# Performance work log

Hardware: AMD Instinct MI355X
Metric: run time of the kernel (lower is better)

The kernel has to match this reference:

```python
import jax, jax.numpy as jnp
import numpy as np
from jax import lax

B, N, C = 4, 16384, 256
NH, HD = 8, 32          # num_heads, head_dim
SR = 4                  # spatial reduction ratio
LMAX = 6144             # max per-batch query length (static pad size)
QLENS = np.array([2048, 6144, 3072, 5120], dtype=np.int32)
TQ = int(QLENS.sum())   # 16384 total ragged queries
SCALE = HD ** -0.5


def setup_inputs() -> dict:
    key = jax.random.key(0)
    ks = jax.random.split(key, 6)
    w = lambda k, s: jax.random.normal(k, s, jnp.float32) * 0.02
    return {
        "x": jax.random.normal(ks[0], (B, N, C), jnp.float32),
        "q": jax.random.normal(ks[1], (TQ, C), jnp.float32),
        "H": 128,
        "W": 128,
        "q_lengths": jnp.asarray(QLENS),
        "w_q": w(ks[2], (C, C)),        # stored [in, out] (= torch W.T)
        "w_kv": w(ks[3], (C, 2 * C)),
        "sr_w": w(ks[4], (C, C, SR, SR)),  # OIHW
        "sr_b": jnp.zeros((C,), jnp.float32),
        "ln_g": jnp.ones((C,), jnp.float32),
        "ln_b": jnp.zeros((C,), jnp.float32),
        "proj_w": w(ks[5], (C, C)),
        "proj_b": jnp.zeros((C,), jnp.float32),
    }


def reference(x, q, H, W, q_lengths, w_q, w_kv, sr_w, sr_b, ln_g, ln_b, proj_w, proj_b):
    # q projection -> per-head ragged queries [NH, TQ, HD]
    qh = (q @ w_q).reshape(TQ, NH, HD).transpose(1, 0, 2)

    # spatial reduction of KV source: conv(k=SR, stride=SR) + LayerNorm
    x_ = x.transpose(0, 2, 1).reshape(B, C, H, W)
    x_ = lax.conv_general_dilated(x_, sr_w, (SR, SR), "VALID",
                                  dimension_numbers=("NCHW", "OIHW", "NCHW"))
    x_ = x_ + sr_b[None, :, None, None]
    x_ = x_.reshape(B, C, -1).transpose(0, 2, 1)  # [B, Nkv, C]
    mu = x_.mean(-1, keepdims=True)
    var = ((x_ - mu) ** 2).mean(-1, keepdims=True)
    x_ = (x_ - mu) * lax.rsqrt(var + 1e-5) * ln_g + ln_b

    # kv projection -> [NH, B, Nkv, HD] each
    kv = (x_ @ w_kv).reshape(B, -1, 2, NH, HD)
    k = kv[:, :, 0].transpose(2, 0, 1, 3)
    v = kv[:, :, 1].transpose(2, 0, 1, 3)

    # ragged -> padded layout for the variable-length attention
    batch_ids = jnp.repeat(jnp.arange(B), q_lengths, total_repeat_length=TQ)
    offsets = jnp.cumsum(q_lengths) - q_lengths
    pos = jnp.arange(TQ) - offsets[batch_ids]
    qp = jnp.zeros((NH, B, LMAX, HD), qh.dtype).at[:, batch_ids, pos].set(qh)

    # per-batch attention over reduced keys (padded rows are discarded below)
    attn = jax.nn.softmax(jnp.einsum("hbld,hbkd->hblk", qp, k) * SCALE, axis=-1)
    op = jnp.einsum("hblk,hbkd->hbld", attn, v)

    # gather valid ragged outputs back: [NH, TQ, HD] -> [TQ, C]
    o = op[:, batch_ids, pos].transpose(1, 0, 2).reshape(TQ, C)
    return o @ proj_w + proj_b
```

## Files before the change

### kernel.cpp

```cpp
#include <hip/hip_runtime.h>
#include <hip/hip_bf16.h>


using bf16 = __hip_bfloat16;
using f32x4 = __attribute__((ext_vector_type(4))) float;
using bf16x8 = __attribute__((ext_vector_type(8))) short;

#define DEVINL __device__ __forceinline__
#define AS1 __attribute__((address_space(1)))
#define AS3 __attribute__((address_space(3)))

DEVINL f32x4 mfma16(bf16x8 a, bf16x8 b, f32x4 c) {
    return __builtin_amdgcn_mfma_f32_16x16x32_bf16(a, b, c, 0, 0, 0);
}

DEVINL unsigned short f2bf(float f) {
    union { float f; unsigned u; } x; x.f = f;
    unsigned u = x.u;
    u += 0x7fffu + ((u >> 16) & 1u);
    return (unsigned short)(u >> 16);
}

DEVINL unsigned pk_rtz(float a, float b) {
    return __builtin_amdgcn_perm(__float_as_uint(b), __float_as_uint(a), 0x07060302u);
}

DEVINL float ex2(float x) { return __builtin_amdgcn_exp2f(x); }

DEVINL void gl16(const bf16* g, bf16* l) {
    __builtin_amdgcn_global_load_lds(
        (const AS1 void*)(unsigned long long)(uintptr_t)g,
        (AS3 void*)(unsigned)(uintptr_t)l,
        16, 0, 0);
}


__global__ __launch_bounds__(256) void cast_bf16_kernel(const float* __restrict__ in,
                                                        bf16* __restrict__ out, int n8) {
    int i = blockIdx.x * 256 + threadIdx.x;
    if (i >= n8) return;
    float4 a = ((const float4*)in)[i * 2];
    float4 b = ((const float4*)in)[i * 2 + 1];
    uint4 u;
    u.x = f2bf(a.x) | ((unsigned)f2bf(a.y) << 16);
    u.y = f2bf(a.z) | ((unsigned)f2bf(a.w) << 16);
    u.z = f2bf(b.x) | ((unsigned)f2bf(b.y) << 16);
    u.w = f2bf(b.z) | ((unsigned)f2bf(b.w) << 16);
    ((uint4*)out)[i] = u;
}

__global__ __launch_bounds__(256) void im2col_kernel(const float* __restrict__ x,
                                                     bf16* __restrict__ xim) {
    int m = blockIdx.x * 256 + threadIdx.x;
    int cc8 = (m & 31) << 3;
    int dydx = (m >> 5) & 15;
    int pr = m >> 9;
    int b = pr >> 10, pi = pr & 1023;
    int ii = pi >> 5, jj = pi & 31;
    int dy = dydx >> 2, dx = dydx & 3;
    int pos = ((ii << 2) + dy) * 128 + (jj << 2) + dx;
    const float* s = &x[(size_t)((b << 14) + pos) * 256 + cc8];
    float4 a = *(const float4*)s;
    float4 c = *(const float4*)(s + 4);
    uint4 u;
    u.x = f2bf(a.x) | ((unsigned)f2bf(a.y) << 16);
    u.y = f2bf(a.z) | ((unsigned)f2bf(a.w) << 16);
    u.z = f2bf(c.x) | ((unsigned)f2bf(c.y) << 16);
    u.w = f2bf(c.z) | ((unsigned)f2bf(c.w) << 16);
    *(uint4*)&xim[(size_t)m * 8] = u;
}

__global__ __launch_bounds__(256) void transpose_cast_kernel(const float* __restrict__ in,
                                                             bf16* __restrict__ out, int K, int N) {
    int idx = blockIdx.x * 256 + threadIdx.x;
    if (idx >= K * N) return;
    int k = idx % K, n = idx / K;
    out[idx] = __float2bfloat16(in[k * N + n]);
}

__global__ __launch_bounds__(256) void conv_w_kernel(const float* __restrict__ sr_w,
                                                     bf16* __restrict__ out) {
    int idx = blockIdx.x * 256 + threadIdx.x;
    int o = idx >> 12, rest = idx & 4095, dydx = rest >> 8, c = rest & 255;
    out[idx] = __float2bfloat16(sr_w[((o << 8) + c) * 16 + dydx]);
}

template<int EMODE>
__global__ __launch_bounds__(256, 4) void gemm_kernel(
    const bf16* __restrict__ A, const bf16* __restrict__ WT,
    const float* __restrict__ bias,
    bf16* __restrict__ outb, float* __restrict__ outf, bf16* __restrict__ out2,
    int M, int N, int K, int KS)
{
    __shared__ alignas(16) bf16 As[2][64 * 64];
    __shared__ alignas(16) bf16 Bs[2][64 * 64];
    const int cpx = gridDim.x >> 3;
    const int bx = (blockIdx.x & 7) * cpx + (blockIdx.x >> 3);
    const int ntn = N >> 6;
    const int tm = bx / ntn, tn = bx % ntn;
    const int tid = threadIdx.x, lane = tid & 63, wid = tid >> 6;
    const int l15 = lane & 15, g = lane >> 4;
    const int wm = (wid >> 1) << 5, wn = (wid & 1) << 5;
    f32x4 acc[2][2] = {};

    int r_[2], cs_[2];
#pragma unroll
    for (int j = 0; j < 2; ++j) {
        int idx = (wid * 2 + j) * 64 + lane;
        r_[j] = idx >> 3;
        cs_[j] = ((idx & 7) ^ (r_[j] & 7)) << 3;
    }
    const bf16* Arow = &A[(size_t)(tm * 64) * K];
    const bf16* Brow = &WT[(size_t)(tn * 64) * K];

    const int kbeg = blockIdx.y * KS;
    const int nsteps = KS >> 6;

    auto stage = [&](int buf, int k0) {
#pragma unroll
        for (int j = 0; j < 2; ++j) {
            gl16(Arow + (size_t)r_[j] * K + (k0 + cs_[j]), &As[buf][(wid * 2 + j) * 512]);
            gl16(Brow + (size_t)r_[j] * K + (k0 + cs_[j]), &Bs[buf][(wid * 2 + j) * 512]);
        }
    };

    stage(0, kbeg);
    __syncthreads();

    for (int t = 0; t < nsteps; ++t) {
        const int buf = t & 1;
        if (t + 1 < nsteps) stage(buf ^ 1, kbeg + (t + 1) * 64);
#pragma unroll
        for (int kk = 0; kk < 2; ++kk) {
            const int sw = l15 & 7;
            const int co = ((kk * 4 + g) ^ sw) << 3;
            bf16x8 a0 = *(const bf16x8*)&As[buf][(wm + l15) * 64 + co];
            bf16x8 a1 = *(const bf16x8*)&As[buf][(wm + 16 + l15) * 64 + co];
            bf16x8 b0 = *(const bf16x8*)&Bs[buf][(wn + l15) * 64 + co];
            bf16x8 b1 = *(const bf16x8*)&Bs[buf][(wn + 16 + l15) * 64 + co];
            acc[0][0] = mfma16(a0, b0, acc[0][0]);
            acc[0][1] = mfma16(a0, b1, acc[0][1]);
            acc[1][0] = mfma16(a1, b0, acc[1][0]);
            acc[1][1] = mfma16(a1, b1, acc[1][1]);
        }
        __syncthreads();
    }

    const float qscale = 0.1767766953f * 1.4426950409f;
#pragma unroll
    for (int mi = 0; mi < 2; ++mi)
#pragma unroll
    for (int ni = 0; ni < 2; ++ni)
#pragma unroll
    for (int r = 0; r < 4; ++r) {
        int row = tm * 64 + wm + mi * 16 + g * 4 + r;
        int col = tn * 64 + wn + ni * 16 + l15;
        float v = acc[mi][ni][r];
        if constexpr (EMODE == 0) {
            outb[(size_t)row * 256 + col] = __float2bfloat16(v * qscale);
        } else if constexpr (EMODE == 1) {
            outf[(size_t)row * 256 + col] = v + bias[col];
        } else if constexpr (EMODE == 2) {
            int bb = row >> 10, key = row & 1023;
            if (col < 256) {
                int hh = col >> 5, d = col & 31;
                outb[(size_t)(((bb << 3) + hh) * 1024 + key) * 32 + d] = __float2bfloat16(v);
            } else {
                int d = col - 256;
                int c = key & 31;
                int pos = (((c >> 2) & 3) << 3) + ((c >> 4) << 2) + (c & 3);
                int keyp = (key & ~31) | pos;
                out2[(size_t)(((bb << 3) + (d >> 5)) * 32 + (d & 31)) * 1024 + keyp] =
                    __float2bfloat16(v);
            }
        } else {
            outf[((size_t)blockIdx.y * 4096 + row) * 256 + col] = v;
        }
    }
}

__global__ __launch_bounds__(256) void ln_kernel(const float* __restrict__ pp,
                                                 const float* __restrict__ cb,
                                                 const float* __restrict__ gw,
                                                 const float* __restrict__ bw,
                                                 bf16* __restrict__ out) {
    int row = blockIdx.x * 4 + (threadIdx.x >> 6);
    int lane = threadIdx.x & 63;
    const size_t base = (size_t)row * 256 + lane * 4;
    float4 v = *(const float4*)&pp[base];
#pragma unroll
    for (int s = 1; s < 4; ++s) {
        const float4 t = *(const float4*)&pp[(size_t)s * (4096 * 256) + base];
        v.x += t.x; v.y += t.y; v.z += t.z; v.w += t.w;
    }
    const float4 cbv = *(const float4*)&cb[lane * 4];
    v.x += cbv.x; v.y += cbv.y; v.z += cbv.z; v.w += cbv.w;

    float s = v.x + v.y + v.z + v.w;
#pragma unroll
    for (int m = 1; m < 64; m <<= 1) s += __shfl_xor(s, m, 64);
    float mu = s * 0.00390625f;
    float d0 = v.x - mu, d1 = v.y - mu, d2 = v.z - mu, d3 = v.w - mu;
    float qv = d0 * d0 + d1 * d1 + d2 * d2 + d3 * d3;
#pragma unroll
    for (int m = 1; m < 64; m <<= 1) qv += __shfl_xor(qv, m, 64);
    float rstd = rsqrtf(qv * 0.00390625f + 1e-5f);
    const float4 gg = *(const float4*)&gw[lane * 4];
    const float4 bb = *(const float4*)&bw[lane * 4];
    uint2 u;
    u.x = f2bf(d0 * rstd * gg.x + bb.x) | ((unsigned)f2bf(d1 * rstd * gg.y + bb.y) << 16);
    u.y = f2bf(d2 * rstd * gg.z + bb.z) | ((unsigned)f2bf(d3 * rstd * gg.w + bb.w) << 16);
    *(uint2*)&out[(size_t)row * 256 + lane * 4] = u;
}

__global__ __launch_bounds__(256, 4) void attn_kernel(
    const bf16* __restrict__ qh, const bf16* __restrict__ kh,
    const bf16* __restrict__ vt, bf16* __restrict__ obf)
{
    __shared__ alignas(16) bf16 Kl[2][128 * 32];
    __shared__ alignas(16) bf16 Vl[2][32 * 128];
    const int bid = blockIdx.x;
    const int h = bid & 7;
    const int tile = bid >> 3;
    const int row0 = tile << 7;
    const int b = (row0 < 2048) ? 0 : (row0 < 8192) ? 1 : (row0 < 11264) ? 2 : 3;
    const int tid = threadIdx.x, lane = tid & 63, w = tid >> 6;
    const int l15 = lane & 15, g = lane >> 4;
    const int qbase = row0 + (w << 5);
    const int bh = (b << 3) + h;

    bf16x8 qfA = *(const bf16x8*)&qh[(size_t)(qbase + l15) * 256 + h * 32 + g * 8];
    bf16x8 qfB = *(const bf16x8*)&qh[(size_t)(qbase + 16 + l15) * 256 + h * 32 + g * 8];

    bf16x8 ones;
    {
        unsigned ov = (l15 == 0) ? 0x3f803f80u : 0u;
        unsigned* op = (unsigned*)&ones;
        op[0] = ov; op[1] = ov; op[2] = ov; op[3] = ov;
    }

    f32x4 o0A = {0.f,0.f,0.f,0.f}, o1A = o0A, o2A = o0A;
    f32x4 o0B = o0A, o1B = o0A, o2B = o0A;
    const f32x4 z = {0.f, 0.f, 0.f, 0.f};

    const int skey = lane >> 2;
    const int skc  = (lane & 3) ^ (skey & 3);
    const int svd  = lane >> 4;
    const int svc  = lane & 15;
    const bf16* kbase = kh + (size_t)bh * 1024 * 32;
    const bf16* vbase = vt + (size_t)bh * 32 * 1024;

    auto stage = [&](int buf, int kb) {
        if (w < 2) {
#pragma unroll
            for (int jj = 0; jj < 4; ++jj) {
                int j = w * 4 + jj;
                int key = (j << 4) + skey;
                gl16(kbase + (size_t)(kb + key) * 32 + (skc << 3), &Kl[buf][j * 512]);
            }
        } else {
#pragma unroll
            for (int jj = 0; jj < 4; ++jj) {
                int j = (w - 2) * 4 + jj;
                int d = (j << 2) + svd;
                gl16(vbase + (size_t)d * 1024 + kb + ((svc ^ (d & 7)) << 3),
                     &Vl[buf][j * 512]);
            }
        }
    };

    stage(0, 0);
    __syncthreads();

    const int kc = g ^ (l15 & 3);
    const int vsw = l15 & 7;

    for (int t = 0; t < 8; ++t) {
        const int buf = t & 1;
        if (t < 7) stage(buf ^ 1, (t + 1) << 7);
#pragma unroll
        for (int s = 0; s < 4; ++s) {
            bf16x8 k0 = *(const bf16x8*)&Kl[buf][((s << 5) + l15) * 32 + (kc << 3)];
            bf16x8 k1 = *(const bf16x8*)&Kl[buf][((s << 5) + 16 + l15) * 32 + (kc << 3)];
            bf16x8 v0 = *(const bf16x8*)&Vl[buf][(l15 << 7) + ((((s << 2) + g) ^ vsw) << 3)];
            bf16x8 v1 = *(const bf16x8*)&Vl[buf][((16 + l15) << 7) + ((((s << 2) + g) ^ vsw) << 3)];

            f32x4 s0A = mfma16(k0, qfA, z);
            f32x4 s1A = mfma16(k1, qfA, z);
            f32x4 s0B = mfma16(k0, qfB, z);
            f32x4 s1B = mfma16(k1, qfB, z);

            uint4 pAu, pBu;
            pAu.x = pk_rtz(ex2(s0A[0]), ex2(s0A[1]));
            pAu.y = pk_rtz(ex2(s0A[2]), ex2(s0A[3]));
            pAu.z = pk_rtz(ex2(s1A[0]), ex2(s1A[1]));
            pAu.w = pk_rtz(ex2(s1A[2]), ex2(s1A[3]));
            pBu.x = pk_rtz(ex2(s0B[0]), ex2(s0B[1]));
            pBu.y = pk_rtz(ex2(s0B[2]), ex2(s0B[3]));
            pBu.z = pk_rtz(ex2(s1B[0]), ex2(s1B[1]));
            pBu.w = pk_rtz(ex2(s1B[2]), ex2(s1B[3]));
            union { uint4 u; bf16x8 v; } cA, cB;
            cA.u = pAu; cB.u = pBu;

            o0A = mfma16(cA.v, v0, o0A);
            o1A = mfma16(cA.v, v1, o1A);
            o2A = mfma16(cA.v, ones, o2A);
            o0B = mfma16(cB.v, v0, o0B);
            o1B = mfma16(cB.v, v1, o1B);
            o2B = mfma16(cB.v, ones, o2B);
        }
        __syncthreads();
    }

#pragma unroll
    for (int r = 0; r < 4; ++r) {
        float invA = 1.f / __shfl(o2A[r], g << 4, 64);
        float invB = 1.f / __shfl(o2B[r], g << 4, 64);
        size_t orowA = (size_t)(qbase + (g << 2) + r) * 256 + h * 32;
        size_t orowB = (size_t)(qbase + 16 + (g << 2) + r) * 256 + h * 32;
        obf[orowA + l15]      = __float2bfloat16(o0A[r] * invA);
        obf[orowA + 16 + l15] = __float2bfloat16(o1A[r] * invA);
        obf[orowB + l15]      = __float2bfloat16(o0B[r] * invB);
        obf[orowB + 16 + l15] = __float2bfloat16(o1B[r] * invB);
    }
}


extern "C" void kernel_launch(void* const* d_in, const int* in_sizes, int n_in,
                              void* d_out, int out_size, void* d_ws, size_t ws_size,
                              hipStream_t stream)
{
    const float* x      = (const float*)d_in[0];
    const float* q      = (const float*)d_in[1];
    const float* w_q    = (const float*)d_in[5];
    const float* w_kv   = (const float*)d_in[6];
    const float* sr_w   = (const float*)d_in[7];
    const float* sr_b   = (const float*)d_in[8];
    const float* ln_g   = (const float*)d_in[9];
    const float* ln_b   = (const float*)d_in[10];
    const float* proj_w = (const float*)d_in[11];
    const float* proj_b = (const float*)d_in[12];

    char* w = (char*)d_ws;
    bf16* xim  = (bf16*)(w + 0);
    bf16* q_bf = (bf16*)(w + 33554432);
    bf16* qh   = (bf16*)(w + 41943040);
    bf16* wqT  = (bf16*)(w + 50331648);
    bf16* wkvT = (bf16*)(w + 50462720);
    bf16* wprT = (bf16*)(w + 50724864);
    bf16* wcv  = (bf16*)(w + 50855936);
    bf16* xln  = (bf16*)(w + 52953088);
    bf16* kh   = (bf16*)(w + 55050240);
    bf16* vt   = (bf16*)(w + 57147392);
    bf16* obf  = (bf16*)(w + 59244544);
    float* partials = (float*)d_out;
    float* out = (float*)d_out;

    transpose_cast_kernel<<<256, 256, 0, stream>>>(w_q, wqT, 256, 256);
    transpose_cast_kernel<<<512, 256, 0, stream>>>(w_kv, wkvT, 256, 512);
    transpose_cast_kernel<<<256, 256, 0, stream>>>(proj_w, wprT, 256, 256);
    conv_w_kernel<<<4096, 256, 0, stream>>>(sr_w, wcv);
    cast_bf16_kernel<<<2048, 256, 0, stream>>>(q, q_bf, 524288);
    im2col_kernel<<<8192, 256, 0, stream>>>(x, xim);

    gemm_kernel<0><<<1024, 256, 0, stream>>>(q_bf, wqT, nullptr, qh, nullptr, nullptr,
                                             16384, 256, 256, 256);
    gemm_kernel<3><<<dim3(256, 4), 256, 0, stream>>>(xim, wcv, nullptr, nullptr, partials,
                                                     nullptr, 4096, 256, 4096, 1024);
    ln_kernel<<<1024, 256, 0, stream>>>(partials, sr_b, ln_g, ln_b, xln);
    gemm_kernel<2><<<512, 256, 0, stream>>>(xln, wkvT, nullptr, kh, nullptr, vt,
                                            4096, 512, 256, 256);
    attn_kernel<<<1024, 256, 0, stream>>>(qh, kh, vt, obf);
    gemm_kernel<1><<<1024, 256, 0, stream>>>(obf, wprT, proj_b, nullptr, out, nullptr,
                                             16384, 256, 256, 256);
}
```

Baseline: 109.6 us.

## Replace split-K conv GEMM with in-block split-K reduction kernel

The conv-as-GEMM no longer launches four split-K blocks that write fp32 partials to global memory for the LayerNorm kernel to sum. A new 1024-thread kernel gives each of four wave groups one quarter of K, reduces the group results in shared memory, adds the conv bias and writes a single fp32 result. This removes the partial-sum global traffic and the extra reads in LN. In exchange it launches only 256 blocks with large shared-memory use, which lowers occupancy and parallelism, and it adds a shared-memory reduction step.

```diff
diff --git a/kernel.cpp b/kernel.cpp
--- a/kernel.cpp
+++ b/kernel.cpp
@@ -173,28 +173,103 @@
                 out2[(size_t)(((bb << 3) + (d >> 5)) * 32 + (d & 31)) * 1024 + keyp] =
                     __float2bfloat16(v);
             }
-        } else {
-            outf[((size_t)blockIdx.y * 4096 + row) * 256 + col] = v;
-        }
-    }
-}
-
-__global__ __launch_bounds__(256) void ln_kernel(const float* __restrict__ pp,
-                                                 const float* __restrict__ cb,
+        }
+    }
+}
+
+__global__ __launch_bounds__(1024, 4) void conv_gemm_kernel(
+    const bf16* __restrict__ A, const bf16* __restrict__ WT,
+    const float* __restrict__ bias, float* __restrict__ outf)
+{
+    __shared__ alignas(16) bf16 As[4][2][64 * 64];
+    __shared__ alignas(16) bf16 Bs[4][2][64 * 64];
+    const int K = 4096;
+    const int bx = (blockIdx.x & 7) * 32 + (blockIdx.x >> 3);
+    const int tm = bx >> 2, tn = bx & 3;
+    const int tid = threadIdx.x, lane = tid & 63, wid = tid >> 6;
+    const int grp = wid >> 2, wg = wid & 3;
+    const int l15 = lane & 15, g = lane >> 4;
+    const int wm = (wg >> 1) << 5, wn = (wg & 1) << 5;
+    f32x4 acc[2][2] = {};
+
+    int r_[2], cs_[2];
+#pragma unroll
+    for (int j = 0; j < 2; ++j) {
+        int idx = (wg * 2 + j) * 64 + lane;
+        r_[j] = idx >> 3;
+        cs_[j] = ((idx & 7) ^ (r_[j] & 7)) << 3;
+    }
+    const bf16* Arow = &A[(size_t)(tm * 64) * K];
+    const bf16* Brow = &WT[(size_t)(tn * 64) * K];
+    const int kbeg = grp << 10;
+
+    auto stage = [&](int buf, int k0) {
+#pragma unroll
+        for (int j = 0; j < 2; ++j) {
+            gl16(Arow + (size_t)r_[j] * K + (k0 + cs_[j]), &As[grp][buf][(wg * 2 + j) * 512]);
+            gl16(Brow + (size_t)r_[j] * K + (k0 + cs_[j]), &Bs[grp][buf][(wg * 2 + j) * 512]);
+        }
+    };
+
+    stage(0, kbeg);
+    __syncthreads();
+
+    for (int t = 0; t < 16; ++t) {
+        const int buf = t & 1;
+        if (t < 15) stage(buf ^ 1, kbeg + (t + 1) * 64);
+#pragma unroll
+        for (int kk = 0; kk < 2; ++kk) {
+            const int sw = l15 & 7;
+            const int co = ((kk * 4 + g) ^ sw) << 3;
+            bf16x8 a0 = *(const bf16x8*)&As[grp][buf][(wm + l15) * 64 + co];
+            bf16x8 a1 = *(const bf16x8*)&As[grp][buf][(wm + 16 + l15) * 64 + co];
+            bf16x8 b0 = *(const bf16x8*)&Bs[grp][buf][(wn + l15) * 64 + co];
+            bf16x8 b1 = *(const bf16x8*)&Bs[grp][buf][(wn + 16 + l15) * 64 + co];
+            acc[0][0] = mfma16(a0, b0, acc[0][0]);
+            acc[0][1] = mfma16(a0, b1, acc[0][1]);
+            acc[1][0] = mfma16(a1, b0, acc[1][0]);
+            acc[1][1] = mfma16(a1, b1, acc[1][1]);
+        }
+        __syncthreads();
+    }
+
+    float* red = (float*)&As[0][0][0];
+#pragma unroll
+    for (int mi = 0; mi < 2; ++mi)
+#pragma unroll
+    for (int ni = 0; ni < 2; ++ni)
+#pragma unroll
+    for (int r = 0; r < 4; ++r) {
+        int row = wm + mi * 16 + g * 4 + r;
+        int col = wn + ni * 16 + l15;
+        red[(grp << 12) + row * 64 + col] = acc[mi][ni][r];
+    }
+    __syncthreads();
+
+    {
+        const int e = tid << 2;
+        float4 s = *(const float4*)&red[e];
+        const float4 s1 = *(const float4*)&red[4096 + e];
+        const float4 s2 = *(const float4*)&red[8192 + e];
+        const float4 s3 = *(const float4*)&red[12288 + e];
+        s.x += s1.x + s2.x + s3.x;
+        s.y += s1.y + s2.y + s3.y;
+        s.z += s1.z + s2.z + s3.z;
+        s.w += s1.w + s2.w + s3.w;
+        const int row = e >> 6, col = e & 63;
+        const float4 bv = *(const float4*)&bias[tn * 64 + col];
+        s.x += bv.x; s.y += bv.y; s.z += bv.z; s.w += bv.w;
+        *(float4*)&outf[(size_t)(tm * 64 + row) * 256 + tn * 64 + col] = s;
+    }
+}
+
+__global__ __launch_bounds__(256) void ln_kernel(const float* __restrict__ xr,
                                                  const float* __restrict__ gw,
                                                  const float* __restrict__ bw,
                                                  bf16* __restrict__ out) {
     int row = blockIdx.x * 4 + (threadIdx.x >> 6);
     int lane = threadIdx.x & 63;
-    const size_t base = (size_t)row * 256 + lane * 4;
-    float4 v = *(const float4*)&pp[base];
-#pragma unroll
-    for (int s = 1; s < 4; ++s) {
-        const float4 t = *(const float4*)&pp[(size_t)s * (4096 * 256) + base];
-        v.x += t.x; v.y += t.y; v.z += t.z; v.w += t.w;
-    }
-    const float4 cbv = *(const float4*)&cb[lane * 4];
-    v.x += cbv.x; v.y += cbv.y; v.z += cbv.z; v.w += cbv.w;
+    const float4 v = *(const float4*)&xr[(size_t)row * 256 + lane * 4];
 
     float s = v.x + v.y + v.z + v.w;
 #pragma unroll
@@ -353,7 +428,7 @@
     bf16* kh   = (bf16*)(w + 55050240);
     bf16* vt   = (bf16*)(w + 57147392);
     bf16* obf  = (bf16*)(w + 59244544);
-    float* partials = (float*)d_out;
+    float* xr  = (float*)(w + 67633152);
     float* out = (float*)d_out;
 
     transpose_cast_kernel<<<256, 256, 0, stream>>>(w_q, wqT, 256, 256);
@@ -365,9 +440,8 @@
 
     gemm_kernel<0><<<1024, 256, 0, stream>>>(q_bf, wqT, nullptr, qh, nullptr, nullptr,
                                              16384, 256, 256, 256);
-    gemm_kernel<3><<<dim3(256, 4), 256, 0, stream>>>(xim, wcv, nullptr, nullptr, partials,
-                                                     nullptr, 4096, 256, 4096, 1024);
-    ln_kernel<<<1024, 256, 0, stream>>>(partials, sr_b, ln_g, ln_b, xln);
+    conv_gemm_kernel<<<256, 1024, 0, stream>>>(xim, wcv, sr_b, xr);
+    ln_kernel<<<1024, 256, 0, stream>>>(xr, ln_g, ln_b, xln);
     gemm_kernel<2><<<512, 256, 0, stream>>>(xln, wkvT, nullptr, kh, nullptr, vt,
                                             4096, 512, 256, 256);
     attn_kernel<<<1024, 256, 0, stream>>>(qh, kh, vt, obf);
```

Result: no change. 109.5 us (-0.1%).

## Fuse im2col into conv GEMM with in-block split-K and merge prep kernels

Applied to the files above, without the earlier changes.

Drops the separate im2col pass. The conv GEMM now loads fp32 x straight into LDS using implicit im2col addressing and converts to bf16 on the fly. Split-K moves from four grid slices with global partials to two groups inside a 1024-thread block, reduced in LDS with the bias added there, so the ln kernel only normalises. The weight transpose/cast kernels and the q cast are merged into one prep launch, which cuts launch count and a 32MB intermediate write and read, at the cost of doubled fp32 LDS traffic and a heavier block.

```diff
diff --git a/kernel.cpp b/kernel.cpp
--- a/kernel.cpp
+++ b/kernel.cpp
@@ -30,59 +30,49 @@
 DEVINL void gl16(const bf16* g, bf16* l) {
     __builtin_amdgcn_global_load_lds(
         (const AS1 void*)(unsigned long long)(uintptr_t)g,
-        (AS3 void*)(unsigned)(uintptr_t)l,
-        16, 0, 0);
-}
-
-
-__global__ __launch_bounds__(256) void cast_bf16_kernel(const float* __restrict__ in,
-                                                        bf16* __restrict__ out, int n8) {
-    int i = blockIdx.x * 256 + threadIdx.x;
-    if (i >= n8) return;
-    float4 a = ((const float4*)in)[i * 2];
-    float4 b = ((const float4*)in)[i * 2 + 1];
-    uint4 u;
-    u.x = f2bf(a.x) | ((unsigned)f2bf(a.y) << 16);
-    u.y = f2bf(a.z) | ((unsigned)f2bf(a.w) << 16);
-    u.z = f2bf(b.x) | ((unsigned)f2bf(b.y) << 16);
-    u.w = f2bf(b.z) | ((unsigned)f2bf(b.w) << 16);
-    ((uint4*)out)[i] = u;
-}
-
-__global__ __launch_bounds__(256) void im2col_kernel(const float* __restrict__ x,
-                                                     bf16* __restrict__ xim) {
-    int m = blockIdx.x * 256 + threadIdx.x;
-    int cc8 = (m & 31) << 3;
-    int dydx = (m >> 5) & 15;
-    int pr = m >> 9;
-    int b = pr >> 10, pi = pr & 1023;
-    int ii = pi >> 5, jj = pi & 31;
-    int dy = dydx >> 2, dx = dydx & 3;
-    int pos = ((ii << 2) + dy) * 128 + (jj << 2) + dx;
-    const float* s = &x[(size_t)((b << 14) + pos) * 256 + cc8];
-    float4 a = *(const float4*)s;
-    float4 c = *(const float4*)(s + 4);
-    uint4 u;
-    u.x = f2bf(a.x) | ((unsigned)f2bf(a.y) << 16);
-    u.y = f2bf(a.z) | ((unsigned)f2bf(a.w) << 16);
-    u.z = f2bf(c.x) | ((unsigned)f2bf(c.y) << 16);
-    u.w = f2bf(c.z) | ((unsigned)f2bf(c.w) << 16);
-    *(uint4*)&xim[(size_t)m * 8] = u;
-}
-
-__global__ __launch_bounds__(256) void transpose_cast_kernel(const float* __restrict__ in,
-                                                             bf16* __restrict__ out, int K, int N) {
-    int idx = blockIdx.x * 256 + threadIdx.x;
-    if (idx >= K * N) return;
-    int k = idx % K, n = idx / K;
-    out[idx] = __float2bfloat16(in[k * N + n]);
-}
-
-__global__ __launch_bounds__(256) void conv_w_kernel(const float* __restrict__ sr_w,
-                                                     bf16* __restrict__ out) {
-    int idx = blockIdx.x * 256 + threadIdx.x;
-    int o = idx >> 12, rest = idx & 4095, dydx = rest >> 8, c = rest & 255;
-    out[idx] = __float2bfloat16(sr_w[((o << 8) + c) * 16 + dydx]);
+        (AS3 void*)(unsigned)(uintptr_t)l, 16, 0, 0);
+}
+DEVINL void gl16f(const float* g, float* l) {
+    __builtin_amdgcn_global_load_lds(
+        (const AS1 void*)(unsigned long long)(uintptr_t)g,
+        (AS3 void*)(unsigned)(uintptr_t)l, 16, 0, 0);
+}
+
+__global__ __launch_bounds__(256) void prep_kernel(
+    const float* __restrict__ w_q, const float* __restrict__ w_kv,
+    const float* __restrict__ proj_w, const float* __restrict__ sr_w,
+    const float* __restrict__ q,
+    bf16* __restrict__ wqT, bf16* __restrict__ wkvT, bf16* __restrict__ wprT,
+    bf16* __restrict__ wcv, bf16* __restrict__ q_bf)
+{
+    const int bb = blockIdx.x;
+    if (bb < 256) {
+        int idx = bb * 256 + threadIdx.x;
+        int k = idx & 255, n = idx >> 8;
+        wqT[idx] = __float2bfloat16(w_q[k * 256 + n]);
+    } else if (bb < 768) {
+        int idx = (bb - 256) * 256 + threadIdx.x;
+        int k = idx & 255, n = idx >> 8;
+        wkvT[idx] = __float2bfloat16(w_kv[k * 512 + n]);
+    } else if (bb < 1024) {
+        int idx = (bb - 768) * 256 + threadIdx.x;
+        int k = idx & 255, n = idx >> 8;
+        wprT[idx] = __float2bfloat16(proj_w[k * 256 + n]);
+    } else if (bb < 5120) {
+        int idx = (bb - 1024) * 256 + threadIdx.x;
+        int o = idx >> 12, rest = idx & 4095, dydx = rest >> 8, c = rest & 255;
+        wcv[idx] = __float2bfloat16(sr_w[((o << 8) + c) * 16 + dydx]);
+    } else {
+        int i = (bb - 5120) * 256 + threadIdx.x;
+        float4 a = ((const float4*)q)[i * 2];
+        float4 b = ((const float4*)q)[i * 2 + 1];
+        uint4 u;
+        u.x = f2bf(a.x) | ((unsigned)f2bf(a.y) << 16);
+        u.y = f2bf(a.z) | ((unsigned)f2bf(a.w) << 16);
+        u.z = f2bf(b.x) | ((unsigned)f2bf(b.y) << 16);
+        u.w = f2bf(b.z) | ((unsigned)f2bf(b.w) << 16);
+        ((uint4*)q_bf)[i] = u;
+    }
 }
 
 template<int EMODE>
@@ -173,28 +163,109 @@
                 out2[(size_t)(((bb << 3) + (d >> 5)) * 32 + (d & 31)) * 1024 + keyp] =
                     __float2bfloat16(v);
             }
-        } else {
-            outf[((size_t)blockIdx.y * 4096 + row) * 256 + col] = v;
-        }
-    }
-}
-
-__global__ __launch_bounds__(256) void ln_kernel(const float* __restrict__ pp,
-                                                 const float* __restrict__ cb,
+        }
+    }
+}
+
+__global__ __launch_bounds__(1024, 4) void conv_gemm_kernel(
+    const float* __restrict__ X, const bf16* __restrict__ WT,
+    const float* __restrict__ bias, float* __restrict__ outf)
+{
+    __shared__ alignas(16) float Af[2][2][64 * 64];
+    __shared__ alignas(16) bf16 Bs[2][2][64 * 64];
+    const int K = 4096;
+    const int bx = (blockIdx.x & 7) * 32 + (blockIdx.x >> 3);
+    const int tm = bx >> 2, tn = bx & 3;
+    const int tid = threadIdx.x, lane = tid & 63, wid = tid >> 6;
+    const int grp = wid >> 3, wg = wid & 7;
+    const int l15 = lane & 15, g = lane >> 4;
+    const int wm = (wg >> 1) << 4, wn = (wg & 1) << 5;
+    f32x4 acc[2] = {};
+
+    size_t laneoffA[2];
+#pragma unroll
+    for (int j = 0; j < 2; ++j) {
+        int rr = (wg * 2 + j) * 4 + (lane >> 4);
+        int pr = tm * 64 + rr;
+        int b = pr >> 10, pi = pr & 1023;
+        int ii = pi >> 5, jj = pi & 31;
+        int c16 = lane & 15;
+        int c16s = ((((c16 >> 1) ^ (rr & 7)) << 1) | (c16 & 1));
+        laneoffA[j] = ((size_t)((b << 14) + (ii << 2) * 128 + (jj << 2))) * 256
+                      + c16s * 4;
+    }
+    const int rB = wg * 8 + (lane >> 3);
+    const int csB = ((lane & 7) ^ (rB & 7)) << 3;
+    const bf16* BrowP = &WT[(size_t)(tn * 64 + rB) * K + csB];
+
+    const int kbeg = grp << 11;
+
+    auto stage = [&](int buf, int t) {
+        const int k0 = kbeg + t * 64;
+        const int dydx = k0 >> 8;
+        const int stepoff = ((dydx >> 2) * 128 + (dydx & 3)) * 256 + (k0 & 255);
+#pragma unroll
+        for (int j = 0; j < 2; ++j)
+            gl16f(X + laneoffA[j] + stepoff, &Af[grp][buf][(wg * 2 + j) * 256]);
+        gl16(BrowP + k0, &Bs[grp][buf][wg * 512]);
+    };
+
+    stage(0, 0);
+    __syncthreads();
+
+    for (int t = 0; t < 32; ++t) {
+        const int buf = t & 1;
+        if (t + 1 < 32) stage(buf ^ 1, t + 1);
+#pragma unroll
+        for (int kk = 0; kk < 2; ++kk) {
+            const int sw = l15 & 7;
+            const int uo = ((kk * 4 + g) ^ sw) << 3;
+            const float* ap = &Af[grp][buf][(wm + l15) * 64 + uo];
+            float4 lo = *(const float4*)ap;
+            float4 hi = *(const float4*)(ap + 4);
+            uint4 au;
+            au.x = pk_rtz(lo.x, lo.y);  au.y = pk_rtz(lo.z, lo.w);
+            au.z = pk_rtz(hi.x, hi.y);  au.w = pk_rtz(hi.z, hi.w);
+            union { uint4 u; bf16x8 v; } ac; ac.u = au;
+            bf16x8 b0 = *(const bf16x8*)&Bs[grp][buf][(wn + l15) * 64 + uo];
+            bf16x8 b1 = *(const bf16x8*)&Bs[grp][buf][(wn + 16 + l15) * 64 + uo];
+            acc[0] = mfma16(ac.v, b0, acc[0]);
+            acc[1] = mfma16(ac.v, b1, acc[1]);
+        }
+        __syncthreads();
+    }
+
+    {
+        float* red = &Af[grp][0][0];
+#pragma unroll
+        for (int ni = 0; ni < 2; ++ni)
+#pragma unroll
+        for (int r = 0; r < 4; ++r)
+            red[(wm + g * 4 + r) * 64 + wn + ni * 16 + l15] = acc[ni][r];
+    }
+    __syncthreads();
+    {
+        const int e = tid << 2;
+        const float4 s0 = *(const float4*)&Af[0][0][e];
+        const float4 s1 = *(const float4*)&Af[1][0][e];
+        const int row = e >> 6, col = e & 63;
+        const float4 bv = *(const float4*)&bias[tn * 64 + col];
+        float4 o;
+        o.x = s0.x + s1.x + bv.x;
+        o.y = s0.y + s1.y + bv.y;
+        o.z = s0.z + s1.z + bv.z;
+        o.w = s0.w + s1.w + bv.w;
+        *(float4*)&outf[(size_t)(tm * 64 + row) * 256 + tn * 64 + col] = o;
+    }
+}
+
+__global__ __launch_bounds__(256) void ln_kernel(const float* __restrict__ xr,
                                                  const float* __restrict__ gw,
                                                  const float* __restrict__ bw,
                                                  bf16* __restrict__ out) {
     int row = blockIdx.x * 4 + (threadIdx.x >> 6);
     int lane = threadIdx.x & 63;
-    const size_t base = (size_t)row * 256 + lane * 4;
-    float4 v = *(const float4*)&pp[base];
-#pragma unroll
-    for (int s = 1; s < 4; ++s) {
-        const float4 t = *(const float4*)&pp[(size_t)s * (4096 * 256) + base];
-        v.x += t.x; v.y += t.y; v.z += t.z; v.w += t.w;
-    }
-    const float4 cbv = *(const float4*)&cb[lane * 4];
-    v.x += cbv.x; v.y += cbv.y; v.z += cbv.z; v.w += cbv.w;
+    const float4 v = *(const float4*)&xr[(size_t)row * 256 + lane * 4];
 
     float s = v.x + v.y + v.z + v.w;
 #pragma unroll
@@ -342,32 +413,25 @@
     const float* proj_b = (const float*)d_in[12];
 
     char* w = (char*)d_ws;
-    bf16* xim  = (bf16*)(w + 0);
-    bf16* q_bf = (bf16*)(w + 33554432);
-    bf16* qh   = (bf16*)(w + 41943040);
-    bf16* wqT  = (bf16*)(w + 50331648);
-    bf16* wkvT = (bf16*)(w + 50462720);
-    bf16* wprT = (bf16*)(w + 50724864);
-    bf16* wcv  = (bf16*)(w + 50855936);
-    bf16* xln  = (bf16*)(w + 52953088);
-    bf16* kh   = (bf16*)(w + 55050240);
-    bf16* vt   = (bf16*)(w + 57147392);
-    bf16* obf  = (bf16*)(w + 59244544);
-    float* partials = (float*)d_out;
+    bf16* q_bf = (bf16*)(w + 0);
+    bf16* qh   = (bf16*)(w + 8388608);
+    bf16* wqT  = (bf16*)(w + 16777216);
+    bf16* wkvT = (bf16*)(w + 16908288);
+    bf16* wprT = (bf16*)(w + 17170432);
+    bf16* wcv  = (bf16*)(w + 17301504);
+    bf16* xln  = (bf16*)(w + 19398656);
+    bf16* kh   = (bf16*)(w + 21495808);
+    bf16* vt   = (bf16*)(w + 23592960);
+    bf16* obf  = (bf16*)(w + 25690112);
+    float* xr  = (float*)(w + 34078720);
     float* out = (float*)d_out;
 
-    transpose_cast_kernel<<<256, 256, 0, stream>>>(w_q, wqT, 256, 256);
-    transpose_cast_kernel<<<512, 256, 0, stream>>>(w_kv, wkvT, 256, 512);
-    transpose_cast_kernel<<<256, 256, 0, stream>>>(proj_w, wprT, 256, 256);
-    conv_w_kernel<<<4096, 256, 0, stream>>>(sr_w, wcv);
-    cast_bf16_kernel<<<2048, 256, 0, stream>>>(q, q_bf, 524288);
-    im2col_kernel<<<8192, 256, 0, stream>>>(x, xim);
-
+    prep_kernel<<<7168, 256, 0, stream>>>(w_q, w_kv, proj_w, sr_w, q,
+                                          wqT, wkvT, wprT, wcv, q_bf);
     gemm_kernel<0><<<1024, 256, 0, stream>>>(q_bf, wqT, nullptr, qh, nullptr, nullptr,
                                              16384, 256, 256, 256);
-    gemm_kernel<3><<<dim3(256, 4), 256, 0, stream>>>(xim, wcv, nullptr, nullptr, partials,
-                                                     nullptr, 4096, 256, 4096, 1024);
-    ln_kernel<<<1024, 256, 0, stream>>>(partials, sr_b, ln_g, ln_b, xln);
+    conv_gemm_kernel<<<256, 1024, 0, stream>>>(x, wcv, sr_b, xr);
+    ln_kernel<<<1024, 256, 0, stream>>>(xr, ln_g, ln_b, xln);
     gemm_kernel<2><<<512, 256, 0, stream>>>(xln, wkvT, nullptr, kh, nullptr, vt,
                                             4096, 512, 256, 256);
     attn_kernel<<<1024, 256, 0, stream>>>(qh, kh, vt, obf);
```

New measurement: 95.33 us. 13.1% less time.
